# Kernel optimization log

Hardware: AMD Instinct MI355X
Metric: run time of the kernel (lower is better)

## Reference

```python
import jax, jax.numpy as jnp
import numpy as np

N_NODES = 100000
N_EDGES = 1600000
D_FEAT = 48
K = 10
ALPHA = 0.1


def setup_inputs() -> dict:
    key = jax.random.key(0)
    k1, k2, k3 = jax.random.split(key, 3)
    x = jax.random.normal(k1, (N_NODES, D_FEAT), dtype=jnp.float32)
    edge_index = jax.random.randint(k2, (2, N_EDGES), 0, N_NODES, dtype=jnp.int64)
    edge_weight = jax.random.uniform(k3, (N_EDGES,), dtype=jnp.float32)
    return {"x": x, "edge_index": edge_index, "edge_weight": edge_weight}


def reference(x, edge_index, edge_weight):
    row, col = edge_index[0], edge_index[1]
    # degree-weighted normalization: w_ij / sum_j w_ij
    deg_w = jax.ops.segment_sum(edge_weight, row, num_segments=N_NODES)
    norm = edge_weight / (deg_w[row] + 1e-10)  # [E]

    def step(h, _):
        # gather h at source-of-message (col), scale, scatter-add to row
        msg = jax.ops.segment_sum(norm[:, None] * h[col], row, num_segments=N_NODES)
        h_new = (1.0 - ALPHA) * msg + ALPHA * x
        return h_new, None

    h, _ = jax.lax.scan(step, x, None, length=K)
    return h
```

## Files before the change

### kernel.cpp

```cpp
#include <hip/hip_runtime.h>
#include <hip/hip_fp16.h>

#define N_NODES 100000
#define N_EDGES 1600000
#define K_ITER 10

#define TPN 6
#define NPB 32
#define PAD 4
#define CSTRIDE 8

#define SCAN_TB   256
#define SCAN_EPT  8
#define SCAN_SEG  (SCAN_TB * SCAN_EPT)
#define SCAN_NB   ((N_NODES + SCAN_SEG - 1) / SCAN_SEG)

typedef unsigned int u32;

__global__ void k_count(const int* __restrict__ row, u32* __restrict__ cnt,
                        unsigned char* __restrict__ pos_local, int E) {
    int i = blockIdx.x * blockDim.x + threadIdx.x;
    if (i < E) pos_local[i] = (unsigned char)atomicAdd(&cnt[row[i] << 3], 1u);
}

__device__ __forceinline__ int padded_cnt(const u32* cnt, int i) {
    int cv = (int)cnt[i << 3];
    return (cv + (PAD - 1)) & ~(PAD - 1);
}

__global__ void k_scanA(const u32* __restrict__ cnt, int* __restrict__ thread_off,
                        int* __restrict__ blocksum) {
    __shared__ int sh[SCAN_TB];
    int b = blockIdx.x, t = threadIdx.x;
    int base = b * SCAN_SEG + t * SCAN_EPT;
    int s = 0;
#pragma unroll
    for (int j = 0; j < SCAN_EPT; ++j) {
        int i = base + j;
        if (i < N_NODES) s += padded_cnt(cnt, i);
    }
    sh[t] = s;
    __syncthreads();
    for (int off = 1; off < SCAN_TB; off <<= 1) {
        int v = (t >= off) ? sh[t - off] : 0;
        __syncthreads();
        sh[t] += v;
        __syncthreads();
    }
    thread_off[b * SCAN_TB + t] = sh[t] - s;
    if (t == SCAN_TB - 1) blocksum[b] = sh[t];
}

__global__ void k_scanB(const int* __restrict__ blocksum, int* __restrict__ blockoff,
                        int* __restrict__ rowptr) {
    __shared__ int sh[SCAN_TB];
    int t = threadIdx.x;
    int v = (t < SCAN_NB) ? blocksum[t] : 0;
    sh[t] = v;
    __syncthreads();
    for (int off = 1; off < SCAN_TB; off <<= 1) {
        int u = (t >= off) ? sh[t - off] : 0;
        __syncthreads();
        sh[t] += u;
        __syncthreads();
    }
    if (t < SCAN_NB) blockoff[t] = sh[t] - v;
    if (t == SCAN_NB - 1) rowptr[N_NODES] = sh[t];
}

__global__ void k_scanC(const u32* __restrict__ cnt, const int* __restrict__ thread_off,
                        const int* __restrict__ blockoff, int* __restrict__ rowptr) {
    int b = blockIdx.x, t = threadIdx.x;
    int base = b * SCAN_SEG + t * SCAN_EPT;
    int run = blockoff[b] + thread_off[b * SCAN_TB + t];
#pragma unroll
    for (int j = 0; j < SCAN_EPT; ++j) {
        int i = base + j;
        if (i < N_NODES) {
            rowptr[i] = run;
            run += padded_cnt(cnt, i);
        }
    }
}

__global__ void k_fill(const int* __restrict__ row, const int* __restrict__ col,
                       const float* __restrict__ w, const int* __restrict__ rowptr,
                       const unsigned char* __restrict__ pos_local,
                       u32* __restrict__ epack, int E) {
    int i = blockIdx.x * blockDim.x + threadIdx.x;
    if (i < E) {
        int pos = rowptr[row[i]] + (int)pos_local[i];
        epack[pos] = ((u32)col[i] << 15) | (__float_as_uint(w[i]) >> 17);
    }
}

__global__ void k_scale(const int* __restrict__ rowptr, const u32* __restrict__ epack,
                        float* __restrict__ scale) {
    int n = blockIdx.x * blockDim.x + threadIdx.x;
    if (n >= N_NODES) return;
    int beg = rowptr[n], end = rowptr[n + 1];
    float s = 0.f;
    for (int e = beg; e < end; ++e)
        s += __uint_as_float((epack[e] & 0x7fffu) << 17);
    scale[n] = 0.9f / (s + 1e-10f);
}

__global__ void k_x2h(const float4* __restrict__ x, float4* __restrict__ x16) {
    int i = blockIdx.x * blockDim.x + threadIdx.x;
    int n = i / TPN, c = i % TPN;
    if (n >= N_NODES) return;
    float4 a = x[n * 12 + 2 * c], b = x[n * 12 + 2 * c + 1];
    float4 o;
    ((__half2*)&o)[0] = __floats2half2_rn(a.x, a.y);
    ((__half2*)&o)[1] = __floats2half2_rn(a.z, a.w);
    ((__half2*)&o)[2] = __floats2half2_rn(b.x, b.y);
    ((__half2*)&o)[3] = __floats2half2_rn(b.z, b.w);
    x16[(n << 3) + c] = o;
}

#define PFMA(UU, HV, AA, BB)                                                  \
    {                                                                         \
        float wv = __uint_as_float(((UU) & 0x7fffu) << 17) * sc;              \
        float2 f0 = __half22float2(*(__half2*)&HV.x);                         \
        float2 f1 = __half22float2(*(__half2*)&HV.y);                         \
        float2 f2 = __half22float2(*(__half2*)&HV.z);                         \
        float2 f3 = __half22float2(*(__half2*)&HV.w);                         \
        AA.x += wv * f0.x; AA.y += wv * f0.y; AA.z += wv * f1.x; AA.w += wv * f1.y; \
        BB.x += wv * f2.x; BB.y += wv * f2.y; BB.z += wv * f3.x; BB.w += wv * f3.y; \
    }

template <int LAST>
__global__ __launch_bounds__(192) void k_pull(const int* __restrict__ rowptr,
                                              const u32* __restrict__ epack,
                                              const float* __restrict__ scale,
                                              const float4* __restrict__ x,
                                              const float4* __restrict__ src16,
                                              void* __restrict__ dstv) {
    int node = blockIdx.x * NPB + threadIdx.x / TPN;
    int c = threadIdx.x % TPN;
    if (node >= N_NODES) return;
    int beg = rowptr[node], end = rowptr[node + 1];
    float sc = scale[node];
    float4 xa = x[node * 12 + 2 * c], xb = x[node * 12 + 2 * c + 1];
    float4 A0 = make_float4(0.1f * xa.x, 0.1f * xa.y, 0.1f * xa.z, 0.1f * xa.w);
    float4 B0 = make_float4(0.1f * xb.x, 0.1f * xb.y, 0.1f * xb.z, 0.1f * xb.w);
    float4 A1 = make_float4(0, 0, 0, 0), B1 = make_float4(0, 0, 0, 0);
    if (beg < end) {
        uint4 p = *(const uint4*)(epack + beg);
        float4 h0 = src16[((p.x >> 15) << 3) + c];
        float4 h1 = src16[((p.y >> 15) << 3) + c];
        float4 h2 = src16[((p.z >> 15) << 3) + c];
        float4 h3 = src16[((p.w >> 15) << 3) + c];
        for (int e = beg + 4; e < end; e += 4) {
            uint4 pn = *(const uint4*)(epack + e);
            float4 g0 = src16[((pn.x >> 15) << 3) + c];
            float4 g1 = src16[((pn.y >> 15) << 3) + c];
            float4 g2 = src16[((pn.z >> 15) << 3) + c];
            float4 g3 = src16[((pn.w >> 15) << 3) + c];
            PFMA(p.x, h0, A0, B0) PFMA(p.y, h1, A1, B1)
            PFMA(p.z, h2, A0, B0) PFMA(p.w, h3, A1, B1)
            p = pn; h0 = g0; h1 = g1; h2 = g2; h3 = g3;
        }
        PFMA(p.x, h0, A0, B0) PFMA(p.y, h1, A1, B1)
        PFMA(p.z, h2, A0, B0) PFMA(p.w, h3, A1, B1)
    }
    float4 RA = make_float4(A0.x + A1.x, A0.y + A1.y, A0.z + A1.z, A0.w + A1.w);
    float4 RB = make_float4(B0.x + B1.x, B0.y + B1.y, B0.z + B1.z, B0.w + B1.w);
    if (LAST) {
        float4* out = (float4*)dstv;
        out[node * 12 + 2 * c]     = RA;
        out[node * 12 + 2 * c + 1] = RB;
    } else {
        float4 o;
        ((__half2*)&o)[0] = __floats2half2_rn(RA.x, RA.y);
        ((__half2*)&o)[1] = __floats2half2_rn(RA.z, RA.w);
        ((__half2*)&o)[2] = __floats2half2_rn(RB.x, RB.y);
        ((__half2*)&o)[3] = __floats2half2_rn(RB.z, RB.w);
        ((float4*)dstv)[(node << 3) + c] = o;
    }
}

extern "C" void kernel_launch(void* const* d_in, const int* in_sizes, int n_in,
                              void* d_out, int out_size, void* d_ws, size_t ws_size,
                              hipStream_t stream) {
    const float* x  = (const float*)d_in[0];
    const int*   ei = (const int*)d_in[1];
    const float* w  = (const float*)d_in[2];
    const int E = in_sizes[2];
    const int* row = ei;
    const int* col = ei + E;

    char* ws = (char*)d_ws;
    int*           rowptr     = (int*)(ws);
    u32*           epack      = (u32*)(ws + 400016);
    float*         scale      = (float*)(ws + 9600096);
    int*           thread_off = (int*)(ws + 10000096);
    int*           blocksum   = (int*)(ws + 10050272);
    int*           blockoff   = (int*)(ws + 10051296);
    u32*           cntS       = (u32*)(ws + 10052352);
    unsigned char* pos_local  = (unsigned char*)(ws + 13252352);
    float4*        hB16       = (float4*)(ws + 14852352);
    float4*        hA16       = (float4*)d_out;

    const int B = 256;
    const int egrid = (E + B - 1) / B;
    const int ngrid = (N_NODES + B - 1) / B;
    const int pgrid = N_NODES / NPB;
    const int xgrid = (N_NODES * TPN + 191) / 192;

    hipMemsetAsync(cntS, 0, (size_t)N_NODES * CSTRIDE * sizeof(u32), stream);
    hipMemsetAsync(epack, 0, (size_t)(N_EDGES + 3 * N_NODES + 16) * sizeof(u32), stream);
    k_count<<<egrid, B, 0, stream>>>(row, cntS, pos_local, E);
    k_scanA<<<SCAN_NB, SCAN_TB, 0, stream>>>(cntS, thread_off, blocksum);
    k_scanB<<<1, SCAN_TB, 0, stream>>>(blocksum, blockoff, rowptr);
    k_scanC<<<SCAN_NB, SCAN_TB, 0, stream>>>(cntS, thread_off, blockoff, rowptr);
    k_fill <<<egrid, B, 0, stream>>>(row, col, w, rowptr, pos_local, epack, E);
    k_scale<<<ngrid, B, 0, stream>>>(rowptr, epack, scale);
    k_x2h  <<<xgrid, 192, 0, stream>>>((const float4*)x, hA16);

    float4* src = hA16;
    float4* dst = hB16;
    for (int k = 1; k <= K_ITER - 1; ++k) {
        k_pull<0><<<pgrid, NPB * TPN, 0, stream>>>(rowptr, epack, scale,
                                                   (const float4*)x, src, dst);
        float4* t = src; src = dst; dst = t;
    }
    k_pull<1><<<pgrid, NPB * TPN, 0, stream>>>(rowptr, epack, scale,
                                               (const float4*)x, src, d_out);
}
```

Before: 495.3 us.

## Privatize edge-count histogram per XCD with workgroup-scope atomics

```diff
diff --git a/kernel.cpp b/kernel.cpp
--- a/kernel.cpp
+++ b/kernel.cpp
@@ -8,7 +8,7 @@
 #define TPN 6
 #define NPB 32
 #define PAD 4
-#define CSTRIDE 8
+#define NXCD 8
 
 #define SCAN_TB   256
 #define SCAN_EPT  8
@@ -16,19 +16,29 @@
 #define SCAN_NB   ((N_NODES + SCAN_SEG - 1) / SCAN_SEG)
 
 typedef unsigned int u32;
-
-__global__ void k_count(const int* __restrict__ row, u32* __restrict__ cnt,
-                        unsigned char* __restrict__ pos_local, int E) {
+typedef unsigned short u16;
+
+__global__ void k_count(const int* __restrict__ row, u32* __restrict__ hist,
+                        u16* __restrict__ pos_local, int E) {
     int i = blockIdx.x * blockDim.x + threadIdx.x;
-    if (i < E) pos_local[i] = (unsigned char)atomicAdd(&cnt[row[i] << 3], 1u);
-}
-
-__device__ __forceinline__ int padded_cnt(const u32* cnt, int i) {
-    int cv = (int)cnt[i << 3];
-    return (cv + (PAD - 1)) & ~(PAD - 1);
-}
-
-__global__ void k_scanA(const u32* __restrict__ cnt, int* __restrict__ thread_off,
+    if (i >= E) return;
+    u32 x;
+    asm volatile("s_getreg_b32 %0, hwreg(HW_REG_XCC_ID)" : "=s"(x));
+    x &= (NXCD - 1);
+    u32 r = (u32)row[i];
+    u32 lr = __hip_atomic_fetch_add(&hist[x * N_NODES + r], 1u,
+                                    __ATOMIC_RELAXED, __HIP_MEMORY_SCOPE_WORKGROUP);
+    pos_local[i] = (u16)((x << 13) | (lr & 0x1fffu));
+}
+
+__device__ __forceinline__ int padded_cnt(const u32* hist, int i) {
+    int s = 0;
+#pragma unroll
+    for (int x = 0; x < NXCD; ++x) s += (int)hist[x * N_NODES + i];
+    return (s + (PAD - 1)) & ~(PAD - 1);
+}
+
+__global__ void k_scanA(const u32* __restrict__ hist, int* __restrict__ thread_off,
                         int* __restrict__ blocksum) {
     __shared__ int sh[SCAN_TB];
     int b = blockIdx.x, t = threadIdx.x;
@@ -37,7 +47,7 @@
 #pragma unroll
     for (int j = 0; j < SCAN_EPT; ++j) {
         int i = base + j;
-        if (i < N_NODES) s += padded_cnt(cnt, i);
+        if (i < N_NODES) s += padded_cnt(hist, i);
     }
     sh[t] = s;
     __syncthreads();
@@ -68,8 +78,9 @@
     if (t == SCAN_NB - 1) rowptr[N_NODES] = sh[t];
 }
 
-__global__ void k_scanC(const u32* __restrict__ cnt, const int* __restrict__ thread_off,
-                        const int* __restrict__ blockoff, int* __restrict__ rowptr) {
+__global__ void k_scanC(const u32* __restrict__ hist, const int* __restrict__ thread_off,
+                        const int* __restrict__ blockoff, int* __restrict__ rowptr,
+                        u32* __restrict__ cumoff) {
     int b = blockIdx.x, t = threadIdx.x;
     int base = b * SCAN_SEG + t * SCAN_EPT;
     int run = blockoff[b] + thread_off[b * SCAN_TB + t];
@@ -78,18 +89,25 @@
         int i = base + j;
         if (i < N_NODES) {
             rowptr[i] = run;
-            run += padded_cnt(cnt, i);
+            int acc = run;
+#pragma unroll
+            for (int x = 0; x < NXCD; ++x) {
+                cumoff[x * N_NODES + i] = (u32)acc;
+                acc += (int)hist[x * N_NODES + i];
+            }
+            run += ((acc - run) + (PAD - 1)) & ~(PAD - 1);
         }
     }
 }
 
 __global__ void k_fill(const int* __restrict__ row, const int* __restrict__ col,
-                       const float* __restrict__ w, const int* __restrict__ rowptr,
-                       const unsigned char* __restrict__ pos_local,
+                       const float* __restrict__ w, const u32* __restrict__ cumoff,
+                       const u16* __restrict__ pos_local,
                        u32* __restrict__ epack, int E) {
     int i = blockIdx.x * blockDim.x + threadIdx.x;
     if (i < E) {
-        int pos = rowptr[row[i]] + (int)pos_local[i];
+        u32 pl = pos_local[i];
+        int pos = (int)cumoff[(pl >> 13) * N_NODES + (u32)row[i]] + (int)(pl & 0x1fffu);
         epack[pos] = ((u32)col[i] << 15) | (__float_as_uint(w[i]) >> 17);
     }
 }
@@ -191,16 +209,17 @@
     const int* col = ei + E;
 
     char* ws = (char*)d_ws;
-    int*           rowptr     = (int*)(ws);
-    u32*           epack      = (u32*)(ws + 400016);
-    float*         scale      = (float*)(ws + 9600096);
-    int*           thread_off = (int*)(ws + 10000096);
-    int*           blocksum   = (int*)(ws + 10050272);
-    int*           blockoff   = (int*)(ws + 10051296);
-    u32*           cntS       = (u32*)(ws + 10052352);
-    unsigned char* pos_local  = (unsigned char*)(ws + 13252352);
-    float4*        hB16       = (float4*)(ws + 14852352);
-    float4*        hA16       = (float4*)d_out;
+    int*    rowptr     = (int*)(ws);
+    u32*    epack      = (u32*)(ws + 400016);
+    float*  scale      = (float*)(ws + 8000096);
+    int*    thread_off = (int*)(ws + 8400096);
+    int*    blocksum   = (int*)(ws + 8450272);
+    int*    blockoff   = (int*)(ws + 8451296);
+    u32*    hist       = (u32*)(ws + 8452352);
+    u32*    cumoff     = (u32*)(ws + 11652352);
+    u16*    pos_local  = (u16*)(ws + 14852352);
+    float4* hB16       = (float4*)(ws + 14852352);
+    float4* hA16       = (float4*)d_out;
 
     const int B = 256;
     const int egrid = (E + B - 1) / B;
@@ -208,13 +227,13 @@
     const int pgrid = N_NODES / NPB;
     const int xgrid = (N_NODES * TPN + 191) / 192;
 
-    hipMemsetAsync(cntS, 0, (size_t)N_NODES * CSTRIDE * sizeof(u32), stream);
+    hipMemsetAsync(hist, 0, (size_t)N_NODES * NXCD * sizeof(u32), stream);
     hipMemsetAsync(epack, 0, (size_t)(N_EDGES + 3 * N_NODES + 16) * sizeof(u32), stream);
-    k_count<<<egrid, B, 0, stream>>>(row, cntS, pos_local, E);
-    k_scanA<<<SCAN_NB, SCAN_TB, 0, stream>>>(cntS, thread_off, blocksum);
+    k_count<<<egrid, B, 0, stream>>>(row, hist, pos_local, E);
+    k_scanA<<<SCAN_NB, SCAN_TB, 0, stream>>>(hist, thread_off, blocksum);
     k_scanB<<<1, SCAN_TB, 0, stream>>>(blocksum, blockoff, rowptr);
-    k_scanC<<<SCAN_NB, SCAN_TB, 0, stream>>>(cntS, thread_off, blockoff, rowptr);
-    k_fill <<<egrid, B, 0, stream>>>(row, col, w, rowptr, pos_local, epack, E);
+    k_scanC<<<SCAN_NB, SCAN_TB, 0, stream>>>(hist, thread_off, blockoff, rowptr, cumoff);
+    k_fill <<<egrid, B, 0, stream>>>(row, col, w, cumoff, pos_local, epack, E);
     k_scale<<<ngrid, B, 0, stream>>>(rowptr, epack, scale);
     k_x2h  <<<xgrid, 192, 0, stream>>>((const float4*)x, hA16);
 
```

Result: slower. 515.4 us (+4.1%).

## Replace global atomic CSR build with two-level shared-memory bucket sort

Applied to the files above, without the earlier changes.

```diff
diff --git a/kernel.cpp b/kernel.cpp
--- a/kernel.cpp
+++ b/kernel.cpp
@@ -8,101 +8,133 @@
 #define TPN 6
 #define NPB 32
 #define PAD 4
-#define CSTRIDE 8
-
-#define SCAN_TB   256
-#define SCAN_EPT  8
-#define SCAN_SEG  (SCAN_TB * SCAN_EPT)
-#define SCAN_NB   ((N_NODES + SCAN_SEG - 1) / SCAN_SEG)
+
+#define NBUCK 391
+#define BROWS 256
+#define BSTRIDE 4608
+#define BK_TB 512
+#define BK_EPT 16
+#define BK_SEG (BK_TB * BK_EPT)
+#define BK_NB ((N_EDGES + BK_SEG - 1) / BK_SEG)
 
 typedef unsigned int u32;
-
-__global__ void k_count(const int* __restrict__ row, u32* __restrict__ cnt,
-                        unsigned char* __restrict__ pos_local, int E) {
-    int i = blockIdx.x * blockDim.x + threadIdx.x;
-    if (i < E) pos_local[i] = (unsigned char)atomicAdd(&cnt[row[i] << 3], 1u);
-}
-
-__device__ __forceinline__ int padded_cnt(const u32* cnt, int i) {
-    int cv = (int)cnt[i << 3];
-    return (cv + (PAD - 1)) & ~(PAD - 1);
-}
-
-__global__ void k_scanA(const u32* __restrict__ cnt, int* __restrict__ thread_off,
-                        int* __restrict__ blocksum) {
-    __shared__ int sh[SCAN_TB];
+typedef unsigned long long u64;
+
+__global__ __launch_bounds__(BK_TB) void k_bucket(const int* __restrict__ row,
+        const int* __restrict__ col, const float* __restrict__ w,
+        u32* __restrict__ bcursor, u64* __restrict__ bedge, int E) {
+    __shared__ u32 hcnt[NBUCK], sbase[NBUCK];
+    int t = threadIdx.x;
+    for (int b = t; b < NBUCK; b += BK_TB) hcnt[b] = 0;
+    __syncthreads();
+    int i0 = blockIdx.x * BK_SEG + t;
+#pragma unroll
+    for (int k = 0; k < BK_EPT; ++k) {
+        int i = i0 + k * BK_TB;
+        if (i < E) atomicAdd(&hcnt[((u32)row[i]) >> 8], 1u);
+    }
+    __syncthreads();
+    for (int b = t; b < NBUCK; b += BK_TB) {
+        u32 c = hcnt[b];
+        sbase[b] = c ? atomicAdd(&bcursor[b], c) : 0u;
+        hcnt[b] = 0;
+    }
+    __syncthreads();
+#pragma unroll
+    for (int k = 0; k < BK_EPT; ++k) {
+        int i = i0 + k * BK_TB;
+        if (i < E) {
+            u32 r = (u32)row[i];
+            u32 b = r >> 8;
+            u32 rk = atomicAdd(&hcnt[b], 1u);
+            u32 idx = sbase[b] + rk;
+            if (idx < BSTRIDE)
+                bedge[(u64)b * BSTRIDE + idx] =
+                    ((u64)(r & 255u) << 32) | ((u64)(u32)col[i] << 15) |
+                    (u64)(__float_as_uint(w[i]) >> 17);
+        }
+    }
+}
+
+__global__ __launch_bounds__(BROWS) void k_buildA(const u32* __restrict__ bcursor,
+        const u64* __restrict__ bedge, u32* __restrict__ cntarr,
+        u32* __restrict__ bsum) {
+    __shared__ u32 cnt[BROWS];
+    __shared__ u32 sh[BROWS];
     int b = blockIdx.x, t = threadIdx.x;
-    int base = b * SCAN_SEG + t * SCAN_EPT;
-    int s = 0;
-#pragma unroll
-    for (int j = 0; j < SCAN_EPT; ++j) {
-        int i = base + j;
-        if (i < N_NODES) s += padded_cnt(cnt, i);
-    }
-    sh[t] = s;
-    __syncthreads();
-    for (int off = 1; off < SCAN_TB; off <<= 1) {
-        int v = (t >= off) ? sh[t - off] : 0;
-        __syncthreads();
-        sh[t] += v;
-        __syncthreads();
-    }
-    thread_off[b * SCAN_TB + t] = sh[t] - s;
-    if (t == SCAN_TB - 1) blocksum[b] = sh[t];
-}
-
-__global__ void k_scanB(const int* __restrict__ blocksum, int* __restrict__ blockoff,
-                        int* __restrict__ rowptr) {
-    __shared__ int sh[SCAN_TB];
+    cnt[t] = 0;
+    __syncthreads();
+    u32 cb = bcursor[b];
+    if (cb > BSTRIDE) cb = BSTRIDE;
+    const u64* be = bedge + (u64)b * BSTRIDE;
+    for (u32 j = t; j < cb; j += BROWS)
+        atomicAdd(&cnt[(u32)(be[j] >> 32) & 255u], 1u);
+    __syncthreads();
+    u32 c = cnt[t];
+    cntarr[b * BROWS + t] = c;
+    sh[t] = (c + PAD - 1) & ~(u32)(PAD - 1);
+    __syncthreads();
+    for (int off = 128; off > 0; off >>= 1) {
+        if (t < off) sh[t] += sh[t + off];
+        __syncthreads();
+    }
+    if (t == 0) bsum[b] = sh[0];
+}
+
+__global__ void k_scanbk(const u32* __restrict__ bsum, u32* __restrict__ bbase,
+                         int* __restrict__ rowptr) {
+    __shared__ u32 sh[512];
     int t = threadIdx.x;
-    int v = (t < SCAN_NB) ? blocksum[t] : 0;
+    u32 v = (t < NBUCK) ? bsum[t] : 0;
     sh[t] = v;
     __syncthreads();
-    for (int off = 1; off < SCAN_TB; off <<= 1) {
-        int u = (t >= off) ? sh[t - off] : 0;
+    for (int off = 1; off < 512; off <<= 1) {
+        u32 u = (t >= off) ? sh[t - off] : 0;
         __syncthreads();
         sh[t] += u;
         __syncthreads();
     }
-    if (t < SCAN_NB) blockoff[t] = sh[t] - v;
-    if (t == SCAN_NB - 1) rowptr[N_NODES] = sh[t];
-}
-
-__global__ void k_scanC(const u32* __restrict__ cnt, const int* __restrict__ thread_off,
-                        const int* __restrict__ blockoff, int* __restrict__ rowptr) {
+    if (t < NBUCK) bbase[t] = sh[t] - v;
+    if (t == NBUCK - 1) rowptr[N_NODES] = (int)sh[t];
+}
+
+__global__ __launch_bounds__(BROWS) void k_buildB(const u32* __restrict__ bcursor,
+        const u64* __restrict__ bedge, const u32* __restrict__ cntarr,
+        const u32* __restrict__ bbase, int* __restrict__ rowptr,
+        u32* __restrict__ epack, float* __restrict__ scale) {
+    __shared__ u32 sh[BROWS];
+    __shared__ u32 run[BROWS];
+    __shared__ float swsum[BROWS];
     int b = blockIdx.x, t = threadIdx.x;
-    int base = b * SCAN_SEG + t * SCAN_EPT;
-    int run = blockoff[b] + thread_off[b * SCAN_TB + t];
-#pragma unroll
-    for (int j = 0; j < SCAN_EPT; ++j) {
-        int i = base + j;
-        if (i < N_NODES) {
-            rowptr[i] = run;
-            run += padded_cnt(cnt, i);
-        }
-    }
-}
-
-__global__ void k_fill(const int* __restrict__ row, const int* __restrict__ col,
-                       const float* __restrict__ w, const int* __restrict__ rowptr,
-                       const unsigned char* __restrict__ pos_local,
-                       u32* __restrict__ epack, int E) {
-    int i = blockIdx.x * blockDim.x + threadIdx.x;
-    if (i < E) {
-        int pos = rowptr[row[i]] + (int)pos_local[i];
-        epack[pos] = ((u32)col[i] << 15) | (__float_as_uint(w[i]) >> 17);
-    }
-}
-
-__global__ void k_scale(const int* __restrict__ rowptr, const u32* __restrict__ epack,
-                        float* __restrict__ scale) {
-    int n = blockIdx.x * blockDim.x + threadIdx.x;
-    if (n >= N_NODES) return;
-    int beg = rowptr[n], end = rowptr[n + 1];
-    float s = 0.f;
-    for (int e = beg; e < end; ++e)
-        s += __uint_as_float((epack[e] & 0x7fffu) << 17);
-    scale[n] = 0.9f / (s + 1e-10f);
+    u32 c = cntarr[b * BROWS + t];
+    u32 p = (c + PAD - 1) & ~(u32)(PAD - 1);
+    sh[t] = p;
+    __syncthreads();
+    for (int off = 1; off < BROWS; off <<= 1) {
+        u32 u = (t >= off) ? sh[t - off] : 0;
+        __syncthreads();
+        sh[t] += u;
+        __syncthreads();
+    }
+    u32 my = bbase[b] + sh[t] - p;
+    int grow = b * BROWS + t;
+    if (grow < N_NODES) rowptr[grow] = (int)my;
+    run[t] = my;
+    swsum[t] = 0.f;
+    __syncthreads();
+    u32 cb = bcursor[b];
+    if (cb > BSTRIDE) cb = BSTRIDE;
+    const u64* be = bedge + (u64)b * BSTRIDE;
+    for (u32 j = t; j < cb; j += BROWS) {
+        u64 e = be[j];
+        u32 r = (u32)(e >> 32) & 255u;
+        u32 pk = (u32)e;
+        u32 pos = atomicAdd(&run[r], 1u);
+        epack[pos] = pk;
+        atomicAdd(&swsum[r], __uint_as_float((pk & 0x7fffu) << 17));
+    }
+    __syncthreads();
+    if (grow < N_NODES) scale[grow] = 0.9f / (swsum[t] + 1e-10f);
 }
 
 __global__ void k_x2h(const float4* __restrict__ x, float4* __restrict__ x16) {
@@ -191,31 +223,27 @@
     const int* col = ei + E;
 
     char* ws = (char*)d_ws;
-    int*           rowptr     = (int*)(ws);
-    u32*           epack      = (u32*)(ws + 400016);
-    float*         scale      = (float*)(ws + 9600096);
-    int*           thread_off = (int*)(ws + 10000096);
-    int*           blocksum   = (int*)(ws + 10050272);
-    int*           blockoff   = (int*)(ws + 10051296);
-    u32*           cntS       = (u32*)(ws + 10052352);
-    unsigned char* pos_local  = (unsigned char*)(ws + 13252352);
-    float4*        hB16       = (float4*)(ws + 14852352);
-    float4*        hA16       = (float4*)d_out;
-
-    const int B = 256;
-    const int egrid = (E + B - 1) / B;
-    const int ngrid = (N_NODES + B - 1) / B;
+    int*    rowptr  = (int*)(ws);
+    float*  scale   = (float*)(ws + 400032);
+    u32*    bsum    = (u32*)(ws + 800032);
+    u32*    bbase   = (u32*)(ws + 801600);
+    u32*    bcursor = (u32*)(ws + 803168);
+    u32*    cntarr  = (u32*)(ws + 804736);
+    u32*    epack   = (u32*)(ws + 1205120);
+    u64*    bedge   = (u64*)(ws + 8805184);
+    float4* hB16    = (float4*)(ws + 14852352);
+    float4* hA16    = (float4*)d_out;
+
     const int pgrid = N_NODES / NPB;
     const int xgrid = (N_NODES * TPN + 191) / 192;
 
-    hipMemsetAsync(cntS, 0, (size_t)N_NODES * CSTRIDE * sizeof(u32), stream);
+    hipMemsetAsync(bcursor, 0, NBUCK * sizeof(u32), stream);
     hipMemsetAsync(epack, 0, (size_t)(N_EDGES + 3 * N_NODES + 16) * sizeof(u32), stream);
-    k_count<<<egrid, B, 0, stream>>>(row, cntS, pos_local, E);
-    k_scanA<<<SCAN_NB, SCAN_TB, 0, stream>>>(cntS, thread_off, blocksum);
-    k_scanB<<<1, SCAN_TB, 0, stream>>>(blocksum, blockoff, rowptr);
-    k_scanC<<<SCAN_NB, SCAN_TB, 0, stream>>>(cntS, thread_off, blockoff, rowptr);
-    k_fill <<<egrid, B, 0, stream>>>(row, col, w, rowptr, pos_local, epack, E);
-    k_scale<<<ngrid, B, 0, stream>>>(rowptr, epack, scale);
+    k_bucket<<<BK_NB, BK_TB, 0, stream>>>(row, col, w, bcursor, bedge, E);
+    k_buildA<<<NBUCK, BROWS, 0, stream>>>(bcursor, bedge, cntarr, bsum);
+    k_scanbk<<<1, 512, 0, stream>>>(bsum, bbase, rowptr);
+    k_buildB<<<NBUCK, BROWS, 0, stream>>>(bcursor, bedge, cntarr, bbase,
+                                          rowptr, epack, scale);
     k_x2h  <<<xgrid, 192, 0, stream>>>((const float4*)x, hA16);
 
     float4* src = hA16;
```

New measurement: 442.8 us. 10.6% less time.
